# Kernel optimization log

Hardware: AMD Instinct MI355X
Metric: run time of the kernel (lower is better)

The kernel has to match this reference:

```python
import jax, jax.numpy as jnp
import numpy as np

B = 64          # batch
NV = 256        # n_vert per rod
CS = [256, 256] # cs_n_vert
N = 3 * NV      # num_nodes
RBC = [100, 200]  # rigid_body_coupling_index
HID = 128


def _build_adjacency():
    A = np.zeros((N, N), dtype=np.float32)
    # chain edges: parent rod, child1 rod, child2 rod (hop=1)
    for i in range(NV - 1):
        A[i, i + 1] = 1; A[i + 1, i] = 1
    for i in range(NV, NV + CS[0] - 1):
        A[i, i + 1] = 1; A[i + 1, i] = 1
    for i in range(2 * NV, 2 * NV + CS[1] - 1):
        A[i, i + 1] = 1; A[i + 1, i] = 1
    zero_mask = np.all(A == 0, axis=-1).astype(np.float32)  # (N,)
    A = (A + np.eye(N, dtype=np.float32)) * (1.0 - zero_mask)  # broadcast over columns, as in torch
    # rigid-body coupling edges (asymmetric, faithful to the source)
    for i, r in enumerate(RBC):
        base = NV * (i + 1)
        A[base, r - 1] = 1; A[base, r] = 1; A[base, r + 1] = 1
        if i == 0:
            A[r, NV] = 1; A[r, NV + 1] = 1
        else:
            A[r, NV + CS[i - 1]] = 1; A[r, NV + CS[i - 1] + 1] = 1
    return A


def setup_inputs() -> dict:
    key = jax.random.key(0)
    ks = jax.random.split(key, 10)
    dims = [(6, 2 * HID), (2 * HID, HID), (HID, HID), (HID, 3)]  # gcn1..gcn4
    params = {}
    for li, (fi, fo) in enumerate(dims):
        params[f"W{li+1}"] = jax.random.normal(ks[li], (fo, fi), jnp.float32) / np.sqrt(fi)
        params[f"b{li+1}"] = jnp.zeros((fo,), jnp.float32)
    return {
        "x": jax.random.normal(ks[8], (B, N, 6), jnp.float32),
        "inputs": jax.random.normal(ks[9], (B, N, 3), jnp.float32),
        "adjacency": jnp.asarray(_build_adjacency()),
        **params,
        "parent_sel": jnp.array([0, NV - 1], jnp.int32),
        "child1_sel": jnp.array([NV - 1], jnp.int32),
        "child2_sel": jnp.array([NV - 1], jnp.int32),
    }


def _gcn(A_norm, x, W, b):
    # linear then symmetric-normalized dense aggregation
    return jnp.einsum('ij,bjf->bif', A_norm, x @ W.T + b)


def reference(x, inputs, adjacency, W1, b1, W2, b2, W3, b3, W4, b4,
              parent_sel, child1_sel, child2_sel):
    deg = adjacency.sum(axis=-1)
    deg_safe = jnp.where(deg == 0, 1.0, deg)
    d = jnp.where(deg == 0, 0.0, deg_safe ** -0.5)
    A_norm = adjacency * d[:, None] * d[None, :]

    x4 = x.reshape(B, 3, NV, -1)
    in4 = inputs.reshape(B, 3, NV, 3)
    # clamp input positions (first 3 features) at grasped vertices
    x4 = x4.at[:, 0, parent_sel, 0:3].set(in4[:, 0, parent_sel])
    x4 = x4.at[:, 1, child1_sel, 0:3].set(in4[:, 1, child1_sel])
    x4 = x4.at[:, 2, child2_sel, 0:3].set(in4[:, 2, child2_sel])
    h = x4.reshape(B, N, -1)

    h = jax.nn.relu(_gcn(A_norm, h, W1, b1))
    h = jax.nn.relu(_gcn(A_norm, h, W2, b2))
    h = _gcn(A_norm, h, W3, b3)
    out = _gcn(A_norm, h, W4, b4)

    o4 = out.reshape(B, 3, NV, 3)
    o4 = o4.at[:, 0, parent_sel].set(in4[:, 0, parent_sel])
    o4 = o4.at[:, 1, child1_sel].set(in4[:, 1, child1_sel])
    o4 = o4.at[:, 2, child2_sel].set(in4[:, 2, child2_sel])
    return o4.reshape(B, N, 3)
```

## Files before the change

kernel.cpp:

```cpp
#include <hip/hip_runtime.h>
#include <math.h>

#define B_ 64
#define NV_ 256
#define N_ 768
#define MAXNNZ 16
#define M_ (B_ * N_)

typedef unsigned short us8 __attribute__((ext_vector_type(8)));
typedef unsigned short us4 __attribute__((ext_vector_type(4)));
typedef __bf16 bf16x8 __attribute__((ext_vector_type(8)));
typedef float f32x4 __attribute__((ext_vector_type(4)));

__device__ inline float bf2f(unsigned short u) {
    return __uint_as_float(((unsigned int)u) << 16);
}
__device__ inline unsigned short f2bf(float f) {
    unsigned int u = __float_as_uint(f);
    unsigned int r = u + 0x7fffu + ((u >> 16) & 1u);
    return (unsigned short)(r >> 16);
}
__device__ inline bf16x8 ld_bf8(const unsigned short* p) {
    us8 u = *(const us8*)p;
    return __builtin_bit_cast(bf16x8, u);
}


__global__ __launch_bounds__(256) void k_prep(
    const float* __restrict__ A, const float* __restrict__ W2,
    const float* __restrict__ W3, const int* __restrict__ psel, int np,
    const int* __restrict__ c1, int n1, const int* __restrict__ c2, int n2,
    int* __restrict__ cols, float* __restrict__ vals, int* __restrict__ nnzArr,
    float* __restrict__ rowsum, int* __restrict__ clampf,
    unsigned short* __restrict__ W2b, unsigned short* __restrict__ W3b) {
    __shared__ int wc[4][MAXNNZ];
    __shared__ float wa[4][MAXNNZ];
    int blk = blockIdx.x, tid = threadIdx.x;

    if (blk < 192) {
        int wave = tid >> 6, lane = tid & 63;
        int i = blk * 4 + wave;
        int cnt = 0;
        float deg = 0.f;
#pragma unroll
        for (int c0 = 0; c0 < N_; c0 += 64) {
            float a = A[(size_t)i * N_ + c0 + lane];
            deg += a;
            unsigned long long m = __ballot(a != 0.f);
            if (a != 0.f) {
                int pos = cnt + __popcll(m & ((1ull << lane) - 1ull));
                if (pos < MAXNNZ) {
                    wc[wave][pos] = c0 + lane;
                    wa[wave][pos] = a;
                }
            }
            cnt += (int)__popcll(m);
        }
#pragma unroll
        for (int o = 32; o > 0; o >>= 1) deg += __shfl_xor(deg, o);
        float dinv_i = (deg == 0.f) ? 0.f : 1.0f / sqrtf(deg);
        __syncthreads();
        int nn = cnt < MAXNNZ ? cnt : MAXNNZ;
        float rs = 0.f;
        for (int p = 0; p < nn; ++p) {
            int c = wc[wave][p];
            float dc = 0.f;
#pragma unroll
            for (int c0 = 0; c0 < N_; c0 += 64) dc += A[(size_t)c * N_ + c0 + lane];
#pragma unroll
            for (int o = 32; o > 0; o >>= 1) dc += __shfl_xor(dc, o);
            float dinv_c = (dc == 0.f) ? 0.f : 1.0f / sqrtf(dc);
            float v = wa[wave][p] * dinv_i * dinv_c;
            rs += v;
            if (lane == 0) {
                cols[i * MAXNNZ + p] = c;
                vals[i * MAXNNZ + p] = v;
            }
        }
        if (lane == 0) {
            nnzArr[i] = cnt;
            rowsum[i] = rs;
        }
    } else if (blk < 384) {
        int idx = (blk - 192) * 256 + tid;
        if (idx < 128 * 256) W2b[idx] = f2bf(W2[idx]);
        else W3b[idx - 128 * 256] = f2bf(W3[idx - 128 * 256]);
    } else {
        clampf[tid] = 0;
        clampf[tid + 256] = 0;
        clampf[tid + 512] = 0;
        __syncthreads();
        if (tid < np) clampf[psel[tid]] = 1;
        else if (tid - np < n1) clampf[NV_ + c1[tid - np]] = 1;
        else if (tid - np - n1 < n2) clampf[2 * NV_ + c2[tid - np - n1]] = 1;
    }
}


__global__ __launch_bounds__(256) void k_layer12(
    const float* __restrict__ x, const float* __restrict__ inputs,
    const int* __restrict__ cols, const float* __restrict__ vals,
    const int* __restrict__ nnzArr, const int* __restrict__ clampf,
    const float* __restrict__ rowsum, const float* __restrict__ W1,
    const float* __restrict__ b1, const unsigned short* __restrict__ W2b,
    const float* __restrict__ b2, unsigned short* __restrict__ T2) {
    __shared__ float Xs[64][6];
    __shared__ float W1T[6][256];
    __shared__ float b1s[256];

    int tid = threadIdx.x;
    int blk = blockIdx.x;
    int i0 = (blk % 12) * 64;
    int base = (blk / 12) * N_;
    int wave = tid >> 6, lane = tid & 63;
    int lrow = lane & 15, kgrp = lane >> 4;

    for (int t = tid; t < 1536; t += 256) {
        int k = t >> 8, c = t & 255;
        W1T[k][c] = W1[c * 6 + k];
    }
    b1s[tid] = b1[tid];

    for (int t = lane; t < 96; t += 64) {
        int f = t % 6, ro = t / 6;
        int i = i0 + wave * 16 + ro;
        int n = nnzArr[i];
        float s = 0.f;
        for (int k = 0; k < n; ++k) {
            int c = cols[i * MAXNNZ + k];
            float val = (f < 3 && clampf[c]) ? inputs[(size_t)(base + c) * 3 + f]
                                             : x[(size_t)(base + c) * 6 + f];
            s += vals[i * MAXNNZ + k] * val;
        }
        Xs[wave * 16 + ro][f] = s;
    }
    __syncthreads();

    int i = i0 + wave * 16 + lrow;
    size_t g = (size_t)(base + i);
    float rs = rowsum[i];
    float xa[6];
#pragma unroll
    for (int k = 0; k < 6; ++k) xa[k] = Xs[wave * 16 + lrow][k];

    f32x4 acc[8];
#pragma unroll
    for (int j = 0; j < 8; ++j) acc[j] = (f32x4){0.f, 0.f, 0.f, 0.f};

#pragma unroll
    for (int s = 0; s < 8; ++s) {
        int c0 = s * 32 + kgrp * 8;
        float h[8];
        f32x4 bv0 = *(const f32x4*)&b1s[c0];
        f32x4 bv1 = *(const f32x4*)&b1s[c0 + 4];
#pragma unroll
        for (int e = 0; e < 4; ++e) {
            h[e] = rs * bv0[e];
            h[4 + e] = rs * bv1[e];
        }
#pragma unroll
        for (int k = 0; k < 6; ++k) {
            f32x4 w0 = *(const f32x4*)&W1T[k][c0];
            f32x4 w1 = *(const f32x4*)&W1T[k][c0 + 4];
#pragma unroll
            for (int e = 0; e < 4; ++e) {
                h[e] += xa[k] * w0[e];
                h[4 + e] += xa[k] * w1[e];
            }
        }
        us8 o;
#pragma unroll
        for (int e = 0; e < 8; ++e) o[e] = f2bf(fmaxf(h[e], 0.f));
        bf16x8 af = __builtin_bit_cast(bf16x8, o);
#pragma unroll
        for (int j = 0; j < 8; ++j) {
            bf16x8 w = ld_bf8(W2b + (size_t)(j * 16 + lrow) * 256 + c0);
            acc[j] = __builtin_amdgcn_mfma_f32_16x16x32_bf16(w, af, acc[j], 0, 0, 0);
        }
    }

#pragma unroll
    for (int j = 0; j < 8; ++j) {
        f32x4 bv = *(const f32x4*)&b2[j * 16 + kgrp * 4];
        us4 o;
#pragma unroll
        for (int e = 0; e < 4; ++e) o[e] = f2bf(acc[j][e] + bv[e]);
        *(us4*)(T2 + g * 128 + j * 16 + kgrp * 4) = o;
    }
}


__global__ __launch_bounds__(256) void k_layer3s(
    const unsigned short* __restrict__ T2, const int* __restrict__ cols,
    const float* __restrict__ vals, const int* __restrict__ nnzArr,
    const unsigned short* __restrict__ W3b, const float* __restrict__ b3,
    const float* __restrict__ W4, float* __restrict__ S) {
    __shared__ float W4s[128 * 3];

    int tid = threadIdx.x;
    int blk = blockIdx.x;
    int i0 = (blk % 12) * 64;
    int base = (blk / 12) * N_;
    int wave = tid >> 6, lane = tid & 63;
    int lrow = lane & 15, kgrp = lane >> 4;

    for (int t = tid; t < 384; t += 256) {
        int d = t % 3, nfeat = t / 3;
        W4s[t] = W4[d * 128 + nfeat];
    }
    __syncthreads();

    int i = i0 + wave * 16 + lrow;
    size_t g = (size_t)(base + i);
    int n = nnzArr[i];
    if (n > MAXNNZ) n = MAXNNZ;

    float fa[4][8];
#pragma unroll
    for (int s = 0; s < 4; ++s)
#pragma unroll
        for (int e = 0; e < 8; ++e) fa[s][e] = 0.f;

    for (int k = 0; k < n; ++k) {
        int c = cols[i * MAXNNZ + k];
        float v = vals[i * MAXNNZ + k];
        const unsigned short* p = T2 + (size_t)(base + c) * 128 + kgrp * 8;
#pragma unroll
        for (int s = 0; s < 4; ++s) {
            us8 z = *(const us8*)(p + s * 32);
#pragma unroll
            for (int e = 0; e < 8; ++e) fa[s][e] += v * bf2f(z[e]);
        }
    }

    bf16x8 af[4];
#pragma unroll
    for (int s = 0; s < 4; ++s) {
        us8 o;
#pragma unroll
        for (int e = 0; e < 8; ++e) o[e] = f2bf(fmaxf(fa[s][e], 0.f));
        af[s] = __builtin_bit_cast(bf16x8, o);
    }

    f32x4 acc[8];
#pragma unroll
    for (int j = 0; j < 8; ++j) acc[j] = (f32x4){0.f, 0.f, 0.f, 0.f};
#pragma unroll
    for (int s = 0; s < 4; ++s) {
#pragma unroll
        for (int j = 0; j < 8; ++j) {
            bf16x8 w = ld_bf8(W3b + (size_t)(j * 16 + lrow) * 128 + s * 32 + kgrp * 8);
            acc[j] = __builtin_amdgcn_mfma_f32_16x16x32_bf16(w, af[s], acc[j], 0, 0, 0);
        }
    }

    float s0 = 0.f, s1 = 0.f, s2 = 0.f;
#pragma unroll
    for (int j = 0; j < 8; ++j) {
        f32x4 bv = *(const f32x4*)&b3[j * 16 + kgrp * 4];
#pragma unroll
        for (int e = 0; e < 4; ++e) {
            float tv = acc[j][e] + bv[e];
            int nfeat = j * 16 + kgrp * 4 + e;
            s0 += tv * W4s[nfeat * 3 + 0];
            s1 += tv * W4s[nfeat * 3 + 1];
            s2 += tv * W4s[nfeat * 3 + 2];
        }
    }
    s0 += __shfl_xor(s0, 16); s0 += __shfl_xor(s0, 32);
    s1 += __shfl_xor(s1, 16); s1 += __shfl_xor(s1, 32);
    s2 += __shfl_xor(s2, 16); s2 += __shfl_xor(s2, 32);
    if (kgrp == 0) {
        S[g * 3 + 0] = s0;
        S[g * 3 + 1] = s1;
        S[g * 3 + 2] = s2;
    }
}


__global__ __launch_bounds__(256) void k_aggS(const float* __restrict__ S,
                                              const int* __restrict__ cols,
                                              const float* __restrict__ vals,
                                              const int* __restrict__ nnzArr,
                                              float* __restrict__ U) {
    int idx = blockIdx.x * 256 + threadIdx.x;
    if (idx >= M_ * 3) return;
    int f = idx % 3;
    int r = idx / 3;
    int i = r % N_;
    int base = r - i;
    int n = nnzArr[i];
    if (n > MAXNNZ) n = MAXNNZ;
    float s = 0.f;
    for (int k = 0; k < n; ++k) {
        int c = cols[i * MAXNNZ + k];
        s += vals[i * MAXNNZ + k] * S[(size_t)(base + c) * 3 + f];
    }
    U[idx] = s;
}


__global__ __launch_bounds__(256) void k_out(const float* __restrict__ U,
                                             const float* __restrict__ inputs,
                                             const int* __restrict__ cols,
                                             const float* __restrict__ vals,
                                             const int* __restrict__ nnzArr,
                                             const float* __restrict__ rowsum,
                                             const float* __restrict__ b4,
                                             const int* __restrict__ clampf,
                                             float* __restrict__ out) {
    int idx = blockIdx.x * 256 + threadIdx.x;
    if (idx >= M_ * 3) return;
    int f = idx % 3;
    int r = idx / 3;
    int i = r % N_;
    int base = r - i;
    if (clampf[i]) {
        out[idx] = inputs[(size_t)r * 3 + f];
        return;
    }
    int n = nnzArr[i];
    if (n > MAXNNZ) n = MAXNNZ;
    float s = rowsum[i] * b4[f];
    for (int k = 0; k < n; ++k) {
        int c = cols[i * MAXNNZ + k];
        s += vals[i * MAXNNZ + k] * U[(size_t)(base + c) * 3 + f];
    }
    out[idx] = s;
}


extern "C" void kernel_launch(void* const* d_in, const int* in_sizes, int n_in,
                              void* d_out, int out_size, void* d_ws, size_t ws_size,
                              hipStream_t stream) {
    const float* x      = (const float*)d_in[0];
    const float* inputs = (const float*)d_in[1];
    const float* A      = (const float*)d_in[2];
    const float* W1     = (const float*)d_in[3];
    const float* b1     = (const float*)d_in[4];
    const float* W2     = (const float*)d_in[5];
    const float* b2     = (const float*)d_in[6];
    const float* W3     = (const float*)d_in[7];
    const float* b3     = (const float*)d_in[8];
    const float* W4     = (const float*)d_in[9];
    const float* b4     = (const float*)d_in[10];
    const int* psel     = (const int*)d_in[11];
    const int* c1sel    = (const int*)d_in[12];
    const int* c2sel    = (const int*)d_in[13];
    int np = in_sizes[11], n1 = in_sizes[12], n2 = in_sizes[13];
    float* out = (float*)d_out;

    char* ws = (char*)d_ws;
    float* rowsum          = (float*)(ws + 3072);
    int*   nnzA            = (int*)(ws + 6144);
    int*   clampf          = (int*)(ws + 9216);
    int*   cols            = (int*)(ws + 12288);
    float* vals            = (float*)(ws + 61440);
    unsigned short* W2b    = (unsigned short*)(ws + 110592);
    unsigned short* W3b    = (unsigned short*)(ws + 176128);
    float* S               = (float*)(ws + 417792);
    float* U               = (float*)(ws + 1048576);
    unsigned short* T2     = (unsigned short*)(ws + 27144192);

    k_prep<<<385, 256, 0, stream>>>(A, W2, W3, psel, np, c1sel, n1, c2sel, n2,
                                    cols, vals, nnzA, rowsum, clampf, W2b, W3b);

    k_layer12<<<M_ / 64, 256, 0, stream>>>(x, inputs, cols, vals, nnzA, clampf, rowsum,
                                           W1, b1, W2b, b2, T2);
    k_layer3s<<<M_ / 64, 256, 0, stream>>>(T2, cols, vals, nnzA, W3b, b3, W4, S);
    k_aggS<<<(M_ * 3 + 255) / 256, 256, 0, stream>>>(S, cols, vals, nnzA, U);
    k_out<<<(M_ * 3 + 255) / 256, 256, 0, stream>>>(U, inputs, cols, vals, nnzA,
                                                    rowsum, b4, clampf, out);
}
```

Before: 70.09 us.

## Split degree/sparse prep, fuse final two aggregations, remap block order

```diff
diff --git a/kernel.cpp b/kernel.cpp
--- a/kernel.cpp
+++ b/kernel.cpp
@@ -26,61 +26,22 @@
 }
 
 
-__global__ __launch_bounds__(256) void k_prep(
+__global__ __launch_bounds__(256) void k_deg_conv(
     const float* __restrict__ A, const float* __restrict__ W2,
     const float* __restrict__ W3, const int* __restrict__ psel, int np,
     const int* __restrict__ c1, int n1, const int* __restrict__ c2, int n2,
-    int* __restrict__ cols, float* __restrict__ vals, int* __restrict__ nnzArr,
-    float* __restrict__ rowsum, int* __restrict__ clampf,
+    float* __restrict__ dinv, int* __restrict__ clampf,
     unsigned short* __restrict__ W2b, unsigned short* __restrict__ W3b) {
-    __shared__ int wc[4][MAXNNZ];
-    __shared__ float wa[4][MAXNNZ];
     int blk = blockIdx.x, tid = threadIdx.x;
-
     if (blk < 192) {
         int wave = tid >> 6, lane = tid & 63;
         int i = blk * 4 + wave;
-        int cnt = 0;
         float deg = 0.f;
 #pragma unroll
-        for (int c0 = 0; c0 < N_; c0 += 64) {
-            float a = A[(size_t)i * N_ + c0 + lane];
-            deg += a;
-            unsigned long long m = __ballot(a != 0.f);
-            if (a != 0.f) {
-                int pos = cnt + __popcll(m & ((1ull << lane) - 1ull));
-                if (pos < MAXNNZ) {
-                    wc[wave][pos] = c0 + lane;
-                    wa[wave][pos] = a;
-                }
-            }
-            cnt += (int)__popcll(m);
-        }
+        for (int c0 = 0; c0 < N_; c0 += 64) deg += A[(size_t)i * N_ + c0 + lane];
 #pragma unroll
         for (int o = 32; o > 0; o >>= 1) deg += __shfl_xor(deg, o);
-        float dinv_i = (deg == 0.f) ? 0.f : 1.0f / sqrtf(deg);
-        __syncthreads();
-        int nn = cnt < MAXNNZ ? cnt : MAXNNZ;
-        float rs = 0.f;
-        for (int p = 0; p < nn; ++p) {
-            int c = wc[wave][p];
-            float dc = 0.f;
-#pragma unroll
-            for (int c0 = 0; c0 < N_; c0 += 64) dc += A[(size_t)c * N_ + c0 + lane];
-#pragma unroll
-            for (int o = 32; o > 0; o >>= 1) dc += __shfl_xor(dc, o);
-            float dinv_c = (dc == 0.f) ? 0.f : 1.0f / sqrtf(dc);
-            float v = wa[wave][p] * dinv_i * dinv_c;
-            rs += v;
-            if (lane == 0) {
-                cols[i * MAXNNZ + p] = c;
-                vals[i * MAXNNZ + p] = v;
-            }
-        }
-        if (lane == 0) {
-            nnzArr[i] = cnt;
-            rowsum[i] = rs;
-        }
+        if (lane == 0) dinv[i] = (deg == 0.f) ? 0.f : 1.0f / sqrtf(deg);
     } else if (blk < 384) {
         int idx = (blk - 192) * 256 + tid;
         if (idx < 128 * 256) W2b[idx] = f2bf(W2[idx]);
@@ -97,6 +58,42 @@
 }
 
 
+__global__ __launch_bounds__(256) void k_sparse(const float* __restrict__ A,
+                                                const float* __restrict__ dinv,
+                                                int* __restrict__ cols,
+                                                float* __restrict__ vals,
+                                                int* __restrict__ nnzArr,
+                                                float* __restrict__ rowsum) {
+    int wave = threadIdx.x >> 6, lane = threadIdx.x & 63;
+    int i = blockIdx.x * 4 + wave;
+    float di = dinv[i];
+    int cnt = 0;
+    float rs = 0.f;
+#pragma unroll
+    for (int c0 = 0; c0 < N_; c0 += 64) {
+        int c = c0 + lane;
+        float a = A[(size_t)i * N_ + c];
+        unsigned long long m = __ballot(a != 0.f);
+        if (a != 0.f) {
+            float v = a * di * dinv[c];
+            int pos = cnt + __popcll(m & ((1ull << lane) - 1ull));
+            if (pos < MAXNNZ) {
+                cols[i * MAXNNZ + pos] = c;
+                vals[i * MAXNNZ + pos] = v;
+            }
+            rs += v;
+        }
+        cnt += (int)__popcll(m);
+    }
+#pragma unroll
+    for (int o = 32; o > 0; o >>= 1) rs += __shfl_xor(rs, o);
+    if (lane == 0) {
+        nnzArr[i] = cnt;
+        rowsum[i] = rs;
+    }
+}
+
+
 __global__ __launch_bounds__(256) void k_layer12(
     const float* __restrict__ x, const float* __restrict__ inputs,
     const int* __restrict__ cols, const float* __restrict__ vals,
@@ -109,7 +106,7 @@
     __shared__ float b1s[256];
 
     int tid = threadIdx.x;
-    int blk = blockIdx.x;
+    int blk = ((blockIdx.x & 7) * 96) + (blockIdx.x >> 3);
     int i0 = (blk % 12) * 64;
     int base = (blk / 12) * N_;
     int wave = tid >> 6, lane = tid & 63;
@@ -125,6 +122,7 @@
         int f = t % 6, ro = t / 6;
         int i = i0 + wave * 16 + ro;
         int n = nnzArr[i];
+        if (n > MAXNNZ) n = MAXNNZ;
         float s = 0.f;
         for (int k = 0; k < n; ++k) {
             int c = cols[i * MAXNNZ + k];
@@ -198,7 +196,7 @@
     __shared__ float W4s[128 * 3];
 
     int tid = threadIdx.x;
-    int blk = blockIdx.x;
+    int blk = ((blockIdx.x & 7) * 96) + (blockIdx.x >> 3);
     int i0 = (blk % 12) * 64;
     int base = (blk / 12) * N_;
     int wave = tid >> 6, lane = tid & 63;
@@ -278,37 +276,15 @@
 }
 
 
-__global__ __launch_bounds__(256) void k_aggS(const float* __restrict__ S,
+__global__ __launch_bounds__(256) void k_out2(const float* __restrict__ S,
+                                              const float* __restrict__ inputs,
                                               const int* __restrict__ cols,
                                               const float* __restrict__ vals,
                                               const int* __restrict__ nnzArr,
-                                              float* __restrict__ U) {
-    int idx = blockIdx.x * 256 + threadIdx.x;
-    if (idx >= M_ * 3) return;
-    int f = idx % 3;
-    int r = idx / 3;
-    int i = r % N_;
-    int base = r - i;
-    int n = nnzArr[i];
-    if (n > MAXNNZ) n = MAXNNZ;
-    float s = 0.f;
-    for (int k = 0; k < n; ++k) {
-        int c = cols[i * MAXNNZ + k];
-        s += vals[i * MAXNNZ + k] * S[(size_t)(base + c) * 3 + f];
-    }
-    U[idx] = s;
-}
-
-
-__global__ __launch_bounds__(256) void k_out(const float* __restrict__ U,
-                                             const float* __restrict__ inputs,
-                                             const int* __restrict__ cols,
-                                             const float* __restrict__ vals,
-                                             const int* __restrict__ nnzArr,
-                                             const float* __restrict__ rowsum,
-                                             const float* __restrict__ b4,
-                                             const int* __restrict__ clampf,
-                                             float* __restrict__ out) {
+                                              const float* __restrict__ rowsum,
+                                              const float* __restrict__ b4,
+                                              const int* __restrict__ clampf,
+                                              float* __restrict__ out) {
     int idx = blockIdx.x * 256 + threadIdx.x;
     if (idx >= M_ * 3) return;
     int f = idx % 3;
@@ -324,7 +300,14 @@
     float s = rowsum[i] * b4[f];
     for (int k = 0; k < n; ++k) {
         int c = cols[i * MAXNNZ + k];
-        s += vals[i * MAXNNZ + k] * U[(size_t)(base + c) * 3 + f];
+        int nc = nnzArr[c];
+        if (nc > MAXNNZ) nc = MAXNNZ;
+        float u = 0.f;
+        for (int p = 0; p < nc; ++p) {
+            int j = cols[c * MAXNNZ + p];
+            u += vals[c * MAXNNZ + p] * S[(size_t)(base + j) * 3 + f];
+        }
+        s += vals[i * MAXNNZ + k] * u;
     }
     out[idx] = s;
 }
@@ -351,6 +334,7 @@
     float* out = (float*)d_out;
 
     char* ws = (char*)d_ws;
+    float* dinv            = (float*)(ws + 0);
     float* rowsum          = (float*)(ws + 3072);
     int*   nnzA            = (int*)(ws + 6144);
     int*   clampf          = (int*)(ws + 9216);
@@ -359,16 +343,15 @@
     unsigned short* W2b    = (unsigned short*)(ws + 110592);
     unsigned short* W3b    = (unsigned short*)(ws + 176128);
     float* S               = (float*)(ws + 417792);
-    float* U               = (float*)(ws + 1048576);
     unsigned short* T2     = (unsigned short*)(ws + 27144192);
 
-    k_prep<<<385, 256, 0, stream>>>(A, W2, W3, psel, np, c1sel, n1, c2sel, n2,
-                                    cols, vals, nnzA, rowsum, clampf, W2b, W3b);
+    k_deg_conv<<<385, 256, 0, stream>>>(A, W2, W3, psel, np, c1sel, n1, c2sel, n2,
+                                        dinv, clampf, W2b, W3b);
+    k_sparse<<<192, 256, 0, stream>>>(A, dinv, cols, vals, nnzA, rowsum);
 
     k_layer12<<<M_ / 64, 256, 0, stream>>>(x, inputs, cols, vals, nnzA, clampf, rowsum,
                                            W1, b1, W2b, b2, T2);
     k_layer3s<<<M_ / 64, 256, 0, stream>>>(T2, cols, vals, nnzA, W3b, b3, W4, S);
-    k_aggS<<<(M_ * 3 + 255) / 256, 256, 0, stream>>>(S, cols, vals, nnzA, U);
-    k_out<<<(M_ * 3 + 255) / 256, 256, 0, stream>>>(U, inputs, cols, vals, nnzA,
-                                                    rowsum, b4, clampf, out);
-}
+    k_out2<<<(M_ * 3 + 255) / 256, 256, 0, stream>>>(S, inputs, cols, vals, nnzA,
+                                                     rowsum, b4, clampf, out);
+}
```

Measured after the change: 74.24 us. 5.9% more time.
